# Kernel tuning notes

Hardware: AMD Instinct MI355X
Metric: run time of the kernel (lower is better)

## Reference

```python
import jax, jax.numpy as jnp
import numpy as np

NUM_RELATIONS = 8
NUM_BASES = 4
IN_CH, HID, OUT_CH = 128, 64, 64
N_NODES, N_EDGES = 50000, 500000


def rgcn_conv(x, edge_src, edge_dst, edge_type, basis, comp, root, bias):
    """PyG RGCNConv with basis decomposition and per-relation mean aggregation.
    basis: [B, in, out], comp: [R, B], root: [in, out], bias: [out].
    W_r = sum_b comp[r, b] * basis[b]; msg_e = x[src_e] @ W_{type_e};
    aggregate mean over incoming edges per (node, relation), sum over relations,
    then add root transform and bias.
    """
    n = x.shape[0]
    out_dim = basis.shape[2]
    # Project once through all bases: [N, B, out]  (cheap: B=4)
    h = jnp.einsum('ni,bio->nbo', x, basis)
    # Per-edge message: contract gathered basis features with per-edge comp coeffs
    msg = jnp.einsum('eb,ebo->eo', comp[edge_type], h[edge_src])  # [E, out]
    # Mean aggregation per (dst, relation): segment id = dst*R + relation
    seg = edge_dst * NUM_RELATIONS + edge_type
    sums = jax.ops.segment_sum(msg, seg, num_segments=n * NUM_RELATIONS)
    cnt = jax.ops.segment_sum(jnp.ones((msg.shape[0], 1), msg.dtype), seg,
                              num_segments=n * NUM_RELATIONS)
    mean = sums / jnp.maximum(cnt, 1.0)
    agg = mean.reshape(n, NUM_RELATIONS, out_dim).sum(axis=1)
    return agg + x @ root + bias


def setup_inputs() -> dict:
    key = jax.random.key(0)
    ks = jax.random.split(key, 12)
    s1 = 1.0 / np.sqrt(IN_CH)
    s2 = 1.0 / np.sqrt(HID)
    return {
        'x': jax.random.normal(ks[0], (N_NODES, IN_CH), jnp.float32),
        'edge_index': jax.random.randint(ks[1], (2, N_EDGES), 0, N_NODES, jnp.int64),
        'edge_type': jax.random.randint(ks[2], (N_EDGES,), 0, NUM_RELATIONS, jnp.int64),
        'basis1': jax.random.normal(ks[3], (NUM_BASES, IN_CH, HID), jnp.float32) * s1,
        'comp1': jax.random.normal(ks[4], (NUM_RELATIONS, NUM_BASES), jnp.float32) * 0.5,
        'root1': jax.random.normal(ks[5], (IN_CH, HID), jnp.float32) * s1,
        'bias1': jnp.zeros((HID,), jnp.float32),
        'basis2': jax.random.normal(ks[6], (NUM_BASES, HID, OUT_CH), jnp.float32) * s2,
        'comp2': jax.random.normal(ks[7], (NUM_RELATIONS, NUM_BASES), jnp.float32) * 0.5,
        'root2': jax.random.normal(ks[8], (HID, OUT_CH), jnp.float32) * s2,
        'bias2': jnp.zeros((OUT_CH,), jnp.float32),
    }


def reference(x, edge_index, edge_type, basis1, comp1, root1, bias1,
              basis2, comp2, root2, bias2):
    src, dst = edge_index[0], edge_index[1]
    h = rgcn_conv(x, src, dst, edge_type, basis1, comp1, root1, bias1)
    h = jax.nn.relu(h)
    out = rgcn_conv(h, src, dst, edge_type, basis2, comp2, root2, bias2)
    return out
```

## Files before the change

### kernel.cpp

```cpp
#include <hip/hip_runtime.h>
#include <cstddef>

#define NREL 8
#define SCAN_TILE 4096

typedef __bf16 bf16x8 __attribute__((ext_vector_type(8)));
typedef float f32x4 __attribute__((ext_vector_type(4)));

__device__ __forceinline__ unsigned f2bf_u(float f) {
    unsigned u = __float_as_uint(f);
    u += 0x7FFFu + ((u >> 16) & 1u);
    return u >> 16;
}
__device__ __forceinline__ short f2bf(float f) { return (short)f2bf_u(f); }
__device__ __forceinline__ int pack2bf(float lo, float hi) {
    return (int)(f2bf_u(lo) | (f2bf_u(hi) << 16));
}
__device__ __forceinline__ float bfval(unsigned short g) {
    return __uint_as_float((unsigned)g << 16);
}

__global__ __launch_bounds__(256) void hist_kernel(const int* __restrict__ dst,
                                                   const int* __restrict__ et,
                                                   int* __restrict__ cnt8, int E)
{
    int e = blockIdx.x * 256 + threadIdx.x;
    if (e < E) atomicAdd(&cnt8[dst[e] * NREL + et[e]], 1);
}

__global__ __launch_bounds__(256) void scan_part(const int* __restrict__ cnt8,
                                                 int* __restrict__ tsum, int n)
{
    int base = blockIdx.x * SCAN_TILE;
    int s = 0;
    for (int i = threadIdx.x; i < SCAN_TILE; i += 256) {
        int idx = base + i;
        if (idx < n) {
            int4 a = ((const int4*)cnt8)[idx * 2];
            int4 b = ((const int4*)cnt8)[idx * 2 + 1];
            s += a.x + a.y + a.z + a.w + b.x + b.y + b.z + b.w;
        }
    }
    for (int d = 1; d < 64; d <<= 1) s += __shfl_xor(s, d, 64);
    __shared__ int ws[4];
    if ((threadIdx.x & 63) == 0) ws[threadIdx.x >> 6] = s;
    __syncthreads();
    if (threadIdx.x == 0) tsum[blockIdx.x] = ws[0] + ws[1] + ws[2] + ws[3];
}

__global__ void scan_mid(int* __restrict__ tsum, int* __restrict__ offs_n, int nt)
{
    if (threadIdx.x == 0) {
        int run = 0;
        for (int i = 0; i < nt; ++i) { int t = tsum[i]; tsum[i] = run; run += t; }
        *offs_n = run;
    }
}

__global__ __launch_bounds__(256) void scan_final(const int* __restrict__ cnt8,
                                                  const int* __restrict__ tsum,
                                                  int* __restrict__ offs, int n)
{
    const int lane = threadIdx.x & 63, wid = threadIdx.x >> 6;
    int base = blockIdx.x * SCAN_TILE + threadIdx.x * 16;
    int v[16]; int s = 0;
#pragma unroll
    for (int j = 0; j < 16; ++j) {
        int idx = base + j;
        int dv = 0;
        if (idx < n) {
            int4 a = ((const int4*)cnt8)[idx * 2];
            int4 b = ((const int4*)cnt8)[idx * 2 + 1];
            dv = a.x + a.y + a.z + a.w + b.x + b.y + b.z + b.w;
        }
        v[j] = dv; s += dv;
    }
    int inc = s;
    for (int d = 1; d < 64; d <<= 1) {
        int t = __shfl_up(inc, d, 64);
        if (lane >= d) inc += t;
    }
    __shared__ int wsum[4];
    if (lane == 63) wsum[wid] = inc;
    __syncthreads();
    int run = tsum[blockIdx.x] + (inc - s);
    for (int k = 0; k < wid; ++k) run += wsum[k];
#pragma unroll
    for (int j = 0; j < 16; ++j) {
        int idx = base + j;
        if (idx < n) offs[idx] = run;
        run += v[j];
    }
}

__global__ __launch_bounds__(256) void scatter_kernel(const int* __restrict__ src,
                                                      const int* __restrict__ dst,
                                                      const int* __restrict__ et,
                                                      const int* __restrict__ offs,
                                                      int* __restrict__ cursor,
                                                      const int* __restrict__ cnt8,
                                                      int2* __restrict__ edgeP, int E)
{
    int e = blockIdx.x * 256 + threadIdx.x;
    if (e >= E) return;
    int d = dst[e], r = et[e], s = src[e];
    int c = cnt8[d * NREL + r];
    float inv = 1.0f / (float)(c > 1 ? c : 1);
    int pos = offs[d] + atomicAdd(&cursor[d], 1);
    edgeP[pos] = make_int2(s * NREL + r, __float_as_int(inv));
}

template<int K>
__global__ __launch_bounds__(256) void wfrag_kernel(const float* __restrict__ basis,
                                                    const float* __restrict__ root,
                                                    const float* __restrict__ comp,
                                                    short* __restrict__ Wf)
{
    constexpr int NK = K / 32;
    int tid = blockIdx.x * 256 + threadIdx.x;
    if (tid >= 36 * NK * 64) return;
    int lane = tid & 63, slot = tid >> 6;
    int ks = slot % NK, t = slot / NK;
    int kg = lane >> 4, lr = lane & 15;
    int k0 = ks * 32 + kg * 8;
    union { short s[8]; int4 v; } u;
#pragma unroll
    for (int e = 0; e < 8; ++e) {
        int k = k0 + e;
        float v;
        if (t < 32) {
            int rr = t >> 2, ch = (t & 3) * 16 + lr;
            v = comp[rr * 4 + 0] * basis[((size_t)0 * K + k) * 64 + ch]
              + comp[rr * 4 + 1] * basis[((size_t)1 * K + k) * 64 + ch]
              + comp[rr * 4 + 2] * basis[((size_t)2 * K + k) * 64 + ch]
              + comp[rr * 4 + 3] * basis[((size_t)3 * K + k) * 64 + ch];
        } else {
            v = root[(size_t)k * 64 + (t - 32) * 16 + lr];
        }
        u.s[e] = f2bf(v);
    }
    *(int4*)(Wf + (size_t)tid * 8) = u.v;
}

template<int K, bool AF32>
__global__ __launch_bounds__(256) void gemm_mfma(const void* __restrict__ Ap,
                                                 const short* __restrict__ Wf,
                                                 const float* __restrict__ bias,
                                                 short* __restrict__ hr,
                                                 float* __restrict__ yinit, int N)
{
    constexpr int NK = K / 32;
    const int w = threadIdx.x >> 6, lane = threadIdx.x & 63;
    const int kg = lane >> 4, lr = lane & 15;
    const int rt = blockIdx.x * 4 + w;
    const int g0 = blockIdx.y * 3;

    bf16x8 afrag[NK];
    if (AF32) {
        const float* A = (const float*)Ap;
        int arow = rt * 16 + lr;
        int ar = arow < N ? arow : N - 1;
#pragma unroll
        for (int ks = 0; ks < NK; ++ks) {
            const float* ap = A + (size_t)ar * K + ks * 32 + kg * 8;
            float4 a = *(const float4*)ap;
            float4 b = *(const float4*)(ap + 4);
            union { short s[8]; bf16x8 v; } cv;
            cv.s[0] = f2bf(a.x); cv.s[1] = f2bf(a.y); cv.s[2] = f2bf(a.z); cv.s[3] = f2bf(a.w);
            cv.s[4] = f2bf(b.x); cv.s[5] = f2bf(b.y); cv.s[6] = f2bf(b.z); cv.s[7] = f2bf(b.w);
            afrag[ks] = cv.v;
        }
    } else {
        const short* A = (const short*)Ap;
        const short* ap = A + ((size_t)rt * NK * 64 + lane) * 8;
#pragma unroll
        for (int ks = 0; ks < NK; ++ks)
            afrag[ks] = *(const bf16x8*)(ap + ks * 512);
    }

    f32x4 acc[12];
#pragma unroll
    for (int t = 0; t < 12; ++t) acc[t] = (f32x4){0.f, 0.f, 0.f, 0.f};

    const short* bp = Wf + ((size_t)g0 * 4 * NK * 64 + lane) * 8;
#pragma unroll
    for (int tt = 0; tt < 12; ++tt) {
#pragma unroll
        for (int ks = 0; ks < NK; ++ks) {
            bf16x8 bfrag = *(const bf16x8*)(bp + (size_t)(tt * NK + ks) * 512);
            acc[tt] = __builtin_amdgcn_mfma_f32_16x16x32_bf16(afrag[ks], bfrag,
                                                              acc[tt], 0, 0, 0);
        }
    }

    float b0 = bias[lr], b1 = bias[16 + lr], b2 = bias[32 + lr], b3 = bias[48 + lr];

    const int drow0 = rt * 16 + kg * 4;
#pragma unroll
    for (int r = 0; r < 4; ++r) {
        int dr = drow0 + r;
        if (dr >= N) break;
#pragma unroll
        for (int gg = 0; gg < 3; ++gg) {
            int g = g0 + gg;
            if (g < 8) {
                int u0 = pack2bf(acc[gg * 4 + 0][r], acc[gg * 4 + 1][r]);
                int u1 = pack2bf(acc[gg * 4 + 2][r], acc[gg * 4 + 3][r]);
                *(int2*)(hr + (size_t)dr * 512 + g * 64 + lr * 4) = make_int2(u0, u1);
            } else {
                float4 o = make_float4(acc[gg * 4 + 0][r] + b0, acc[gg * 4 + 1][r] + b1,
                                       acc[gg * 4 + 2][r] + b2, acc[gg * 4 + 3][r] + b3);
                *(float4*)(yinit + (size_t)dr * 64 + lr * 4) = o;
            }
        }
    }
}

template<bool BF16OUT>
__global__ __launch_bounds__(256) void agg_kernel(const int* __restrict__ offs,
                                                  const int2* __restrict__ edgeP,
                                                  const short* __restrict__ hr,
                                                  const float* __restrict__ init,
                                                  float* __restrict__ outF,
                                                  short* __restrict__ outB, int N)
{
    const int dst = blockIdx.x * 4 + (threadIdx.x >> 6);
    const int l = threadIdx.x & 63;
    if (dst >= N) return;

    const unsigned short* hp = (const unsigned short*)hr;
    float acc = init[(size_t)dst * 64 + l];
    int e0 = offs[dst], e1 = offs[dst + 1];

    int e = e0;
    for (; e + 3 < e1; e += 4) {
        int2 p0 = edgeP[e],     p1 = edgeP[e + 1];
        int2 p2 = edgeP[e + 2], p3 = edgeP[e + 3];
        unsigned short g0 = hp[(size_t)p0.x * 64 + l];
        unsigned short g1 = hp[(size_t)p1.x * 64 + l];
        unsigned short g2 = hp[(size_t)p2.x * 64 + l];
        unsigned short g3 = hp[(size_t)p3.x * 64 + l];
        acc = fmaf(bfval(g0), __int_as_float(p0.y), acc);
        acc = fmaf(bfval(g1), __int_as_float(p1.y), acc);
        acc = fmaf(bfval(g2), __int_as_float(p2.y), acc);
        acc = fmaf(bfval(g3), __int_as_float(p3.y), acc);
    }
    for (; e < e1; ++e) {
        int2 p0 = edgeP[e];
        unsigned short g0 = hp[(size_t)p0.x * 64 + l];
        acc = fmaf(bfval(g0), __int_as_float(p0.y), acc);
    }

    int tc = (l & 3) * 16 + (l >> 2);
    if (BF16OUT) {
        int rt2 = dst >> 4, lr2 = dst & 15;
        int ks2 = tc >> 5, kg2 = (tc >> 3) & 3, e2 = tc & 7;
        outB[(((size_t)rt2 * 2 + ks2) * 64 + kg2 * 16 + lr2) * 8 + e2] =
            f2bf(fmaxf(acc, 0.f));
    } else {
        outF[(size_t)dst * 64 + tc] = acc;
    }
}

extern "C" void kernel_launch(void* const* d_in, const int* in_sizes, int n_in,
                              void* d_out, int out_size, void* d_ws, size_t ws_size,
                              hipStream_t stream)
{
    const float* x      = (const float*)d_in[0];
    const int*   ei     = (const int*)d_in[1];
    const int*   et     = (const int*)d_in[2];
    const float* basis1 = (const float*)d_in[3];
    const float* comp1  = (const float*)d_in[4];
    const float* root1  = (const float*)d_in[5];
    const float* bias1  = (const float*)d_in[6];
    const float* basis2 = (const float*)d_in[7];
    const float* comp2  = (const float*)d_in[8];
    const float* root2  = (const float*)d_in[9];
    const float* bias2  = (const float*)d_in[10];
    float* out = (float*)d_out;

    const int N = in_sizes[0] / 128;
    const int E = in_sizes[2];
    const int* src  = ei;
    const int* dstp = ei + E;

    const int gblk = (N + 63) / 64;
    const int NT   = gblk * 4;
    const int ablk = (N + 3) / 4;

    char* p = (char*)d_ws;
    auto carve = [&](size_t bytes) -> char* {
        char* q = p; p += (bytes + 255) & ~(size_t)255; return q;
    };
    int*   cursor  = (int*)carve((size_t)N * 4);
    int*   cnt8    = (int*)carve((size_t)N * NREL * 4);
    char*  zend    = p;
    int*   offs    = (int*)carve((size_t)(N + 1) * 4);
    int*   tsum    = (int*)carve(256 * 4);
    int2*  edgeP   = (int2*)carve((size_t)E * 8);
    short* Wf1     = (short*)carve((size_t)36 * 4 * 64 * 8 * 2);
    short* Wf2     = (short*)carve((size_t)36 * 2 * 64 * 8 * 2);
    float* yinit   = (float*)carve((size_t)N * 64 * 4);
    short* xf2     = (short*)carve((size_t)NT * 2 * 64 * 8 * 2);
    short* hr      = (short*)carve((size_t)N * 512 * 2);

    hipMemsetAsync(cursor, 0, (size_t)(zend - (char*)cursor), stream);

    const int ntiles = (N + SCAN_TILE - 1) / SCAN_TILE;

    hist_kernel<<<(E + 255) / 256, 256, 0, stream>>>(dstp, et, cnt8, E);
    scan_part<<<ntiles, 256, 0, stream>>>(cnt8, tsum, N);
    scan_mid<<<1, 64, 0, stream>>>(tsum, offs + N, ntiles);
    scan_final<<<ntiles, 256, 0, stream>>>(cnt8, tsum, offs, N);
    scatter_kernel<<<(E + 255) / 256, 256, 0, stream>>>(src, dstp, et, offs, cursor,
                                                        cnt8, edgeP, E);

    wfrag_kernel<128><<<(36 * 4 * 64 + 255) / 256, 256, 0, stream>>>(basis1, root1, comp1, Wf1);
    wfrag_kernel<64><<<(36 * 2 * 64 + 255) / 256, 256, 0, stream>>>(basis2, root2, comp2, Wf2);

    gemm_mfma<128, true><<<dim3(gblk, 3), 256, 0, stream>>>(x, Wf1, bias1, hr, yinit, N);
    agg_kernel<true><<<ablk, 256, 0, stream>>>(offs, edgeP, hr, yinit, nullptr, xf2, N);

    gemm_mfma<64, false><<<dim3(gblk, 3), 256, 0, stream>>>(xf2, Wf2, bias2, hr, yinit, N);
    agg_kernel<false><<<ablk, 256, 0, stream>>>(offs, edgeP, hr, yinit, out, nullptr, N);
}
```

Baseline: 200.2 us.

## Stage weight fragments in LDS, pre-pack x to bf16, reorder launches

Splits the fp32-to-bf16 conversion of x into a separate afrag_kernel, so the first GEMM reads pre-packed bf16 fragments just like the second layer. The GEMM now copies its block's weight fragments into shared memory once and reads B fragments from LDS instead of from global memory on every MFMA. The memset is replaced by a custom zero kernel, and the first GEMM is launched before the CSR build kernels. The costs are an extra kernel launch, an extra write and read of x in bf16, and LDS use (up to 48KB for K=128), which may limit occupancy.

Result: faster. 192.8 us (-3.7%).

```diff
diff --git a/kernel.cpp b/kernel.cpp
--- a/kernel.cpp
+++ b/kernel.cpp
@@ -18,6 +18,12 @@
 }
 __device__ __forceinline__ float bfval(unsigned short g) {
     return __uint_as_float((unsigned)g << 16);
+}
+
+__global__ __launch_bounds__(256) void zero_kernel(int4* __restrict__ p, int n16)
+{
+    int i = blockIdx.x * 256 + threadIdx.x;
+    if (i < n16) p[i] = make_int4(0, 0, 0, 0);
 }
 
 __global__ __launch_bounds__(256) void hist_kernel(const int* __restrict__ dst,
@@ -142,52 +148,71 @@
     *(int4*)(Wf + (size_t)tid * 8) = u.v;
 }
 
-template<int K, bool AF32>
-__global__ __launch_bounds__(256) void gemm_mfma(const void* __restrict__ Ap,
+template<int K>
+__global__ __launch_bounds__(256) void afrag_kernel(const float* __restrict__ x,
+                                                    short* __restrict__ xf,
+                                                    int N, int NT)
+{
+    constexpr int NK = K / 32;
+    int tid = blockIdx.x * 256 + threadIdx.x;
+    if (tid >= NT * NK * 64) return;
+    int lane = tid & 63, slot = tid >> 6;
+    int ks = slot % NK, rt = slot / NK;
+    int kg = lane >> 4, lr = lane & 15;
+    int row = rt * 16 + lr, k = ks * 32 + kg * 8;
+    union { short s[8]; int4 v; } u;
+    if (row < N) {
+        const float* xp = x + (size_t)row * K + k;
+        float4 a = *(const float4*)xp;
+        float4 b = *(const float4*)(xp + 4);
+        u.s[0] = f2bf(a.x); u.s[1] = f2bf(a.y); u.s[2] = f2bf(a.z); u.s[3] = f2bf(a.w);
+        u.s[4] = f2bf(b.x); u.s[5] = f2bf(b.y); u.s[6] = f2bf(b.z); u.s[7] = f2bf(b.w);
+    } else {
+        u.v = make_int4(0, 0, 0, 0);
+    }
+    *(int4*)(xf + (size_t)tid * 8) = u.v;
+}
+
+template<int K>
+__global__ __launch_bounds__(256) void gemm_mfma(const short* __restrict__ xf,
                                                  const short* __restrict__ Wf,
                                                  const float* __restrict__ bias,
                                                  short* __restrict__ hr,
                                                  float* __restrict__ yinit, int N)
 {
     constexpr int NK = K / 32;
+    __shared__ short lds[12 * NK * 512];
+
     const int w = threadIdx.x >> 6, lane = threadIdx.x & 63;
     const int kg = lane >> 4, lr = lane & 15;
     const int rt = blockIdx.x * 4 + w;
     const int g0 = blockIdx.y * 3;
 
+    {
+        const int4* gsrc = (const int4*)(Wf + (size_t)g0 * 4 * NK * 512);
+        int4* ldst = (int4*)lds;
+#pragma unroll
+        for (int i = threadIdx.x; i < 12 * NK * 64; i += 256)
+            ldst[i] = gsrc[i];
+    }
+
     bf16x8 afrag[NK];
-    if (AF32) {
-        const float* A = (const float*)Ap;
-        int arow = rt * 16 + lr;
-        int ar = arow < N ? arow : N - 1;
+    const short* ap = xf + ((size_t)rt * NK * 64 + lane) * 8;
+#pragma unroll
+    for (int ks = 0; ks < NK; ++ks)
+        afrag[ks] = *(const bf16x8*)(ap + ks * 512);
+
+    f32x4 acc[12];
+#pragma unroll
+    for (int t = 0; t < 12; ++t) acc[t] = (f32x4){0.f, 0.f, 0.f, 0.f};
+
+    __syncthreads();
+
+#pragma unroll
+    for (int tt = 0; tt < 12; ++tt) {
 #pragma unroll
         for (int ks = 0; ks < NK; ++ks) {
-            const float* ap = A + (size_t)ar * K + ks * 32 + kg * 8;
-            float4 a = *(const float4*)ap;
-            float4 b = *(const float4*)(ap + 4);
-            union { short s[8]; bf16x8 v; } cv;
-            cv.s[0] = f2bf(a.x); cv.s[1] = f2bf(a.y); cv.s[2] = f2bf(a.z); cv.s[3] = f2bf(a.w);
-            cv.s[4] = f2bf(b.x); cv.s[5] = f2bf(b.y); cv.s[6] = f2bf(b.z); cv.s[7] = f2bf(b.w);
-            afrag[ks] = cv.v;
-        }
-    } else {
-        const short* A = (const short*)Ap;
-        const short* ap = A + ((size_t)rt * NK * 64 + lane) * 8;
-#pragma unroll
-        for (int ks = 0; ks < NK; ++ks)
-            afrag[ks] = *(const bf16x8*)(ap + ks * 512);
-    }
-
-    f32x4 acc[12];
-#pragma unroll
-    for (int t = 0; t < 12; ++t) acc[t] = (f32x4){0.f, 0.f, 0.f, 0.f};
-
-    const short* bp = Wf + ((size_t)g0 * 4 * NK * 64 + lane) * 8;
-#pragma unroll
-    for (int tt = 0; tt < 12; ++tt) {
-#pragma unroll
-        for (int ks = 0; ks < NK; ++ks) {
-            bf16x8 bfrag = *(const bf16x8*)(bp + (size_t)(tt * NK + ks) * 512);
+            bf16x8 bfrag = *(const bf16x8*)(lds + (tt * NK + ks) * 512 + lane * 8);
             acc[tt] = __builtin_amdgcn_mfma_f32_16x16x32_bf16(afrag[ks], bfrag,
                                                               acc[tt], 0, 0, 0);
         }
@@ -301,12 +326,18 @@
     short* Wf1     = (short*)carve((size_t)36 * 4 * 64 * 8 * 2);
     short* Wf2     = (short*)carve((size_t)36 * 2 * 64 * 8 * 2);
     float* yinit   = (float*)carve((size_t)N * 64 * 4);
+    short* xf1     = (short*)carve((size_t)NT * 4 * 64 * 8 * 2);
     short* xf2     = (short*)carve((size_t)NT * 2 * 64 * 8 * 2);
     short* hr      = (short*)carve((size_t)N * 512 * 2);
 
-    hipMemsetAsync(cursor, 0, (size_t)(zend - (char*)cursor), stream);
-
+    const int zn16 = (int)((zend - (char*)cursor) / 16);
     const int ntiles = (N + SCAN_TILE - 1) / SCAN_TILE;
+
+    zero_kernel<<<(zn16 + 255) / 256, 256, 0, stream>>>((int4*)cursor, zn16);
+    wfrag_kernel<128><<<(36 * 4 * 64 + 255) / 256, 256, 0, stream>>>(basis1, root1, comp1, Wf1);
+    wfrag_kernel<64><<<(36 * 2 * 64 + 255) / 256, 256, 0, stream>>>(basis2, root2, comp2, Wf2);
+    afrag_kernel<128><<<(NT * 4 * 64 + 255) / 256, 256, 0, stream>>>(x, xf1, N, NT);
+    gemm_mfma<128><<<dim3(gblk, 3), 256, 0, stream>>>(xf1, Wf1, bias1, hr, yinit, N);
 
     hist_kernel<<<(E + 255) / 256, 256, 0, stream>>>(dstp, et, cnt8, E);
     scan_part<<<ntiles, 256, 0, stream>>>(cnt8, tsum, N);
@@ -315,12 +346,8 @@
     scatter_kernel<<<(E + 255) / 256, 256, 0, stream>>>(src, dstp, et, offs, cursor,
                                                         cnt8, edgeP, E);
 
-    wfrag_kernel<128><<<(36 * 4 * 64 + 255) / 256, 256, 0, stream>>>(basis1, root1, comp1, Wf1);
-    wfrag_kernel<64><<<(36 * 2 * 64 + 255) / 256, 256, 0, stream>>>(basis2, root2, comp2, Wf2);
-
-    gemm_mfma<128, true><<<dim3(gblk, 3), 256, 0, stream>>>(x, Wf1, bias1, hr, yinit, N);
     agg_kernel<true><<<ablk, 256, 0, stream>>>(offs, edgeP, hr, yinit, nullptr, xf2, N);
 
-    gemm_mfma<64, false><<<dim3(gblk, 3), 256, 0, stream>>>(xf2, Wf2, bias2, hr, yinit, N);
+    gemm_mfma<64><<<dim3(gblk, 3), 256, 0, stream>>>(xf2, Wf2, bias2, hr, yinit, N);
     agg_kernel<false><<<ablk, 256, 0, stream>>>(offs, edgeP, hr, yinit, out, nullptr, N);
 }
```
